# Kernel optimization log

Hardware: AMD Instinct MI355X
Metric: run time of the kernel (lower is better)

## Reference

```python
import jax, jax.numpy as jnp
import numpy as np

INNER_DIM = 512
SCALE = 1.0 / np.sqrt(INNER_DIM).astype(np.float32)  # module scales by 1/sqrt(inner_dim), not head_dim


def setup_inputs() -> dict:
    key = jax.random.key(0)
    ks = jax.random.split(key, 7)
    b, n, d = 4, 4096, 512
    s = 0.02
    return {
        "x": jax.random.normal(ks[0], (b, n, d), jnp.float32),
        "y": jax.random.normal(ks[1], (b, n, d), jnp.float32),
        "Wq": jax.random.normal(ks[2], (INNER_DIM, d), jnp.float32) * s,  # torch Linear weight [out, in]
        "Wk": jax.random.normal(ks[3], (INNER_DIM, d), jnp.float32) * s,
        "Wv": jax.random.normal(ks[4], (INNER_DIM, d), jnp.float32) * s,
        "Wo": jax.random.normal(ks[5], (d, INNER_DIM), jnp.float32) * s,
        "bo": jax.random.normal(ks[6], (d,), jnp.float32) * s,
    }


def reference(x, y, Wq, Wk, Wv, Wo, bo):
    # q, k from x; v from y (bias-free projections)
    q = jnp.einsum('bnd,id->bni', x, Wq)
    k = jnp.einsum('bnd,id->bni', x, Wk)
    v = jnp.einsum('bnd,id->bni', y, Wv)
    # full [b, n, n] scores, scaled by 1/sqrt(inner_dim)
    alpha = jnp.einsum('bik,bjk->bij', q, k) * SCALE
    alpha = jax.nn.softmax(alpha, axis=-1)
    ctx = jnp.einsum('bij,bjd->bid', alpha, v)
    out = jnp.einsum('bid,od->bio', ctx, Wo) + bo
    return out
```

## Files before the change

### kernel.cpp

```cpp
#include <hip/hip_runtime.h>
#include <hip/hip_bf16.h>


typedef unsigned short u16;
typedef __bf16 bf16x8 __attribute__((ext_vector_type(8)));
typedef float f32x4 __attribute__((ext_vector_type(4)));

#define SCALE_QK 0.044194173824159216f

__device__ __forceinline__ u16 f2bf(float f) {
    __hip_bfloat16 h = __float2bfloat16(f);
    return __builtin_bit_cast(u16, h);
}

__device__ __forceinline__ void load_lds16(const void* g, void* l) {
    __builtin_amdgcn_global_load_lds(
        (const __attribute__((address_space(1))) void*)g,
        (__attribute__((address_space(3))) void*)l, 16, 0, 0);
}

__global__ void cvt_bf16_kernel(const float* __restrict__ src, u16* __restrict__ dst,
                                int n8, float scale) {
    int i = blockIdx.x * blockDim.x + threadIdx.x;
    if (i >= n8) return;
    const float4* s4 = (const float4*)src;
    float4 v0 = s4[2 * i], v1 = s4[2 * i + 1];
    union { u16 u[8]; uint4 v; } o;
    o.u[0] = f2bf(v0.x * scale); o.u[1] = f2bf(v0.y * scale);
    o.u[2] = f2bf(v0.z * scale); o.u[3] = f2bf(v0.w * scale);
    o.u[4] = f2bf(v1.x * scale); o.u[5] = f2bf(v1.y * scale);
    o.u[6] = f2bf(v1.z * scale); o.u[7] = f2bf(v1.w * scale);
    ((uint4*)dst)[i] = o.v;
}

__global__ void wvo_kernel(const float* __restrict__ Wo, const float* __restrict__ Wv,
                           float* __restrict__ Wvo) {
    int o = blockIdx.x, t = threadIdx.x;
    float a0 = 0.f, a1 = 0.f;
    for (int i = 0; i < 512; ++i) {
        float w = Wo[o * 512 + i];
        a0 += w * Wv[i * 512 + t];
        a1 += w * Wv[i * 512 + t + 256];
    }
    Wvo[o * 512 + t] = a0;
    Wvo[o * 512 + t + 256] = a1;
}

__global__ void rowsum_kernel(const u16* __restrict__ P, float* __restrict__ l) {
    int row = blockIdx.x * 4 + (threadIdx.x >> 6);
    int lane = threadIdx.x & 63;
    const uint4* base = (const uint4*)(P + (size_t)row * 4096);
    float s = 0.f;
#pragma unroll
    for (int it = 0; it < 8; ++it) {
        uint4 c = base[it * 64 + lane];
        const u16* u = (const u16*)&c;
#pragma unroll
        for (int j = 0; j < 8; ++j)
            s += __uint_as_float(((unsigned)u[j]) << 16);
    }
#pragma unroll
    for (int off = 32; off > 0; off >>= 1) s += __shfl_xor(s, off, 64);
    if (lane == 0) l[row] = s;
}

template <int EPI>
__launch_bounds__(256)
__global__ void gemm_bt_kernel(const u16* __restrict__ A, const u16* __restrict__ B,
                               void* __restrict__ Cout, int N, int K,
                               long long sAz, long long sBz, long long sCz,
                               const float* __restrict__ lvec,
                               const float* __restrict__ bias) {
    __shared__ u16 As[2][128 * 32];
    __shared__ u16 Bs[2][128 * 32];

    const int tid = threadIdx.x;
    const int wave = tid >> 6, lane = tid & 63;
    const int lr = lane & 15, lg = lane >> 4;
    const int wr = wave >> 1, wc = wave & 1;
    const int z = blockIdx.z;
    const int row0 = blockIdx.y * 128, col0 = blockIdx.x * 128;

    const u16* Ab = A + (size_t)z * sAz;
    const u16* Bb = B + (size_t)z * sBz;

    f32x4 acc[4][4];
#pragma unroll
    for (int i = 0; i < 4; ++i)
#pragma unroll
        for (int j = 0; j < 4; ++j) acc[i][j] = (f32x4){0.f, 0.f, 0.f, 0.f};

    const int KT = K >> 5;

#define STAGE(bufi, kt2)                                                          \
    {                                                                             \
        _Pragma("unroll") for (int i = 0; i < 2; ++i) {                           \
            int chunk = i * 256 + tid;                                            \
            int r = chunk >> 2, c4 = chunk & 3;                                   \
            load_lds16(Ab + (size_t)(row0 + r) * K + (kt2) * 32 + c4 * 8,         \
                       &As[bufi][(i * 256 + wave * 64) * 8]);                     \
            load_lds16(Bb + (size_t)(col0 + r) * K + (kt2) * 32 + c4 * 8,         \
                       &Bs[bufi][(i * 256 + wave * 64) * 8]);                     \
        }                                                                         \
    }

    STAGE(0, 0);
    int buf = 0;
    for (int kt = 0; kt < KT; ++kt) {
        __syncthreads();
        if (kt + 1 < KT) STAGE(buf ^ 1, kt + 1);

        bf16x8 af[4], bfr[4];
#pragma unroll
        for (int mf = 0; mf < 4; ++mf)
            af[mf] = *(const bf16x8*)&As[buf][(wr * 64 + mf * 16 + lr) * 32 + lg * 8];
#pragma unroll
        for (int nf = 0; nf < 4; ++nf)
            bfr[nf] = *(const bf16x8*)&Bs[buf][(wc * 64 + nf * 16 + lr) * 32 + lg * 8];
#pragma unroll
        for (int mf = 0; mf < 4; ++mf)
#pragma unroll
            for (int nf = 0; nf < 4; ++nf)
                acc[mf][nf] = __builtin_amdgcn_mfma_f32_16x16x32_bf16(
                    af[mf], bfr[nf], acc[mf][nf], 0, 0, 0);
        buf ^= 1;
    }
#undef STAGE

    const int rbase = row0 + wr * 64;
    const int cbase = col0 + wc * 64;

    if (EPI == 0 || EPI == 2) {
        u16* C = (u16*)Cout + (size_t)z * sCz;
#pragma unroll
        for (int mf = 0; mf < 4; ++mf)
#pragma unroll
            for (int nf = 0; nf < 4; ++nf)
#pragma unroll
                for (int reg = 0; reg < 4; ++reg) {
                    int r = rbase + mf * 16 + lg * 4 + reg;
                    int c = cbase + nf * 16 + lr;
                    float v = acc[mf][nf][reg];
                    if (EPI == 2) v = __expf(v);
                    C[(size_t)r * N + c] = f2bf(v);
                }
    } else if (EPI == 1) {
        u16* C = (u16*)Cout;
#pragma unroll
        for (int mf = 0; mf < 4; ++mf)
#pragma unroll
            for (int nf = 0; nf < 4; ++nf) {
                int rg = rbase + mf * 16 + lg * 4;
                int bsel = rg >> 12, rl = rg & 4095;
                int c = cbase + nf * 16 + lr;
                union { u16 u[4]; uint2 v; } o;
#pragma unroll
                for (int reg = 0; reg < 4; ++reg) o.u[reg] = f2bf(acc[mf][nf][reg]);
                *(uint2*)(C + ((size_t)bsel << 21) + ((size_t)c << 12) + rl) = o.v;
            }
    } else {
        float* C = (float*)Cout + (size_t)z * sCz;
        const float* lz = lvec + z * 4096;
        float bo_c[4];
#pragma unroll
        for (int nf = 0; nf < 4; ++nf) bo_c[nf] = bias[cbase + nf * 16 + lr];
#pragma unroll
        for (int mf = 0; mf < 4; ++mf) {
            float4 lv = *(const float4*)&lz[rbase + mf * 16 + lg * 4];
            float inv[4] = {1.f / lv.x, 1.f / lv.y, 1.f / lv.z, 1.f / lv.w};
#pragma unroll
            for (int nf = 0; nf < 4; ++nf)
#pragma unroll
                for (int reg = 0; reg < 4; ++reg) {
                    int r = rbase + mf * 16 + lg * 4 + reg;
                    int c = cbase + nf * 16 + lr;
                    C[(size_t)r * N + c] = acc[mf][nf][reg] * inv[reg] + bo_c[nf];
                }
        }
    }
}

extern "C" void kernel_launch(void* const* d_in, const int* in_sizes, int n_in,
                              void* d_out, int out_size, void* d_ws, size_t ws_size,
                              hipStream_t stream) {
    const float* x  = (const float*)d_in[0];
    const float* y  = (const float*)d_in[1];
    const float* Wq = (const float*)d_in[2];
    const float* Wk = (const float*)d_in[3];
    const float* Wv = (const float*)d_in[4];
    const float* Wo = (const float*)d_in[5];
    const float* bo = (const float*)d_in[6];
    float* out = (float*)d_out;

    char* ws = (char*)d_ws;
    u16*   xb   = (u16*)(ws + 0);
    u16*   yb   = (u16*)(ws + 16777216);
    u16*   q    = (u16*)(ws + 33554432);
    u16*   k    = (u16*)(ws + 50331648);
    u16*   vwT  = (u16*)(ws + 67108864);
    u16*   Wqb  = (u16*)(ws + 83886080);
    u16*   Wkb  = (u16*)(ws + 84410368);
    u16*   Wvob = (u16*)(ws + 84934656);
    float* Wvo  = (float*)(ws + 85458944);
    float* lsum = (float*)(ws + 86507520);
    u16*   P    = (u16*)(ws + 86573056);

    cvt_bf16_kernel<<<4096, 256, 0, stream>>>(x, xb, 1048576, 1.0f);
    cvt_bf16_kernel<<<4096, 256, 0, stream>>>(y, yb, 1048576, 1.0f);
    cvt_bf16_kernel<<<128, 256, 0, stream>>>(Wq, Wqb, 32768, SCALE_QK);
    cvt_bf16_kernel<<<128, 256, 0, stream>>>(Wk, Wkb, 32768, 1.0f);

    wvo_kernel<<<512, 256, 0, stream>>>(Wo, Wv, Wvo);
    cvt_bf16_kernel<<<128, 256, 0, stream>>>(Wvo, Wvob, 32768, 1.0f);

    gemm_bt_kernel<0><<<dim3(4, 128, 1), 256, 0, stream>>>(xb, Wqb, q, 512, 512,
                                                           0, 0, 0, nullptr, nullptr);
    gemm_bt_kernel<0><<<dim3(4, 128, 1), 256, 0, stream>>>(xb, Wkb, k, 512, 512,
                                                           0, 0, 0, nullptr, nullptr);
    gemm_bt_kernel<1><<<dim3(4, 128, 1), 256, 0, stream>>>(yb, Wvob, vwT, 512, 512,
                                                           0, 0, 0, nullptr, nullptr);

    gemm_bt_kernel<2><<<dim3(32, 32, 4), 256, 0, stream>>>(q, k, P, 4096, 512,
                                                           2097152, 2097152, 16777216,
                                                           nullptr, nullptr);

    rowsum_kernel<<<4096, 256, 0, stream>>>(P, lsum);

    gemm_bt_kernel<3><<<dim3(4, 32, 4), 256, 0, stream>>>(P, vwT, out, 512, 4096,
                                                          16777216, 2097152, 2097152,
                                                          lsum, bo);
}
```

Baseline: 359.6 us.

## Fuse Q/K projections, fold rowsum into PV GEMM, add XCD-aware block remap

```diff
diff --git a/kernel.cpp b/kernel.cpp
--- a/kernel.cpp
+++ b/kernel.cpp
@@ -46,31 +46,11 @@
     Wvo[o * 512 + t + 256] = a1;
 }
 
-__global__ void rowsum_kernel(const u16* __restrict__ P, float* __restrict__ l) {
-    int row = blockIdx.x * 4 + (threadIdx.x >> 6);
-    int lane = threadIdx.x & 63;
-    const uint4* base = (const uint4*)(P + (size_t)row * 4096);
-    float s = 0.f;
-#pragma unroll
-    for (int it = 0; it < 8; ++it) {
-        uint4 c = base[it * 64 + lane];
-        const u16* u = (const u16*)&c;
-#pragma unroll
-        for (int j = 0; j < 8; ++j)
-            s += __uint_as_float(((unsigned)u[j]) << 16);
-    }
-#pragma unroll
-    for (int off = 32; off > 0; off >>= 1) s += __shfl_xor(s, off, 64);
-    if (lane == 0) l[row] = s;
-}
-
 template <int EPI>
 __launch_bounds__(256)
 __global__ void gemm_bt_kernel(const u16* __restrict__ A, const u16* __restrict__ B,
-                               void* __restrict__ Cout, int N, int K,
-                               long long sAz, long long sBz, long long sCz,
-                               const float* __restrict__ lvec,
-                               const float* __restrict__ bias) {
+                               void* __restrict__ Cout, int N, int K, int lda, int ldb,
+                               long long sAz, long long sBz, long long sCz) {
     __shared__ u16 As[2][128 * 32];
     __shared__ u16 Bs[2][128 * 32];
 
@@ -78,8 +58,15 @@
     const int wave = tid >> 6, lane = tid & 63;
     const int lr = lane & 15, lg = lane >> 4;
     const int wr = wave >> 1, wc = wave & 1;
-    const int z = blockIdx.z;
-    const int row0 = blockIdx.y * 128, col0 = blockIdx.x * 128;
+
+    const int gx = gridDim.x, gy = gridDim.y;
+    int bid = (blockIdx.z * gy + blockIdx.y) * gx + blockIdx.x;
+    const int nwg = gx * gy * gridDim.z;
+    int lgc = (bid & 7) * (nwg >> 3) + (bid >> 3);
+    const int bx = lgc % gx;
+    int rem = lgc / gx;
+    const int by = rem % gy, z = rem / gy;
+    const int row0 = by * 128, col0 = bx * 128;
 
     const u16* Ab = A + (size_t)z * sAz;
     const u16* Bb = B + (size_t)z * sBz;
@@ -97,9 +84,9 @@
         _Pragma("unroll") for (int i = 0; i < 2; ++i) {                           \
             int chunk = i * 256 + tid;                                            \
             int r = chunk >> 2, c4 = chunk & 3;                                   \
-            load_lds16(Ab + (size_t)(row0 + r) * K + (kt2) * 32 + c4 * 8,         \
+            load_lds16(Ab + (size_t)(row0 + r) * lda + (kt2) * 32 + c4 * 8,       \
                        &As[bufi][(i * 256 + wave * 64) * 8]);                     \
-            load_lds16(Bb + (size_t)(col0 + r) * K + (kt2) * 32 + c4 * 8,         \
+            load_lds16(Bb + (size_t)(col0 + r) * ldb + (kt2) * 32 + c4 * 8,       \
                        &Bs[bufi][(i * 256 + wave * 64) * 8]);                     \
         }                                                                         \
     }
@@ -144,7 +131,7 @@
                     if (EPI == 2) v = __expf(v);
                     C[(size_t)r * N + c] = f2bf(v);
                 }
-    } else if (EPI == 1) {
+    } else {
         u16* C = (u16*)Cout;
 #pragma unroll
         for (int mf = 0; mf < 4; ++mf)
@@ -158,24 +145,98 @@
                 for (int reg = 0; reg < 4; ++reg) o.u[reg] = f2bf(acc[mf][nf][reg]);
                 *(uint2*)(C + ((size_t)bsel << 21) + ((size_t)c << 12) + rl) = o.v;
             }
-    } else {
-        float* C = (float*)Cout + (size_t)z * sCz;
-        const float* lz = lvec + z * 4096;
-        float bo_c[4];
-#pragma unroll
-        for (int nf = 0; nf < 4; ++nf) bo_c[nf] = bias[cbase + nf * 16 + lr];
-#pragma unroll
-        for (int mf = 0; mf < 4; ++mf) {
-            float4 lv = *(const float4*)&lz[rbase + mf * 16 + lg * 4];
-            float inv[4] = {1.f / lv.x, 1.f / lv.y, 1.f / lv.z, 1.f / lv.w};
-#pragma unroll
-            for (int nf = 0; nf < 4; ++nf)
-#pragma unroll
-                for (int reg = 0; reg < 4; ++reg) {
-                    int r = rbase + mf * 16 + lg * 4 + reg;
-                    int c = cbase + nf * 16 + lr;
-                    C[(size_t)r * N + c] = acc[mf][nf][reg] * inv[reg] + bo_c[nf];
-                }
+    }
+}
+
+__launch_bounds__(512, 4)
+__global__ void pv_kernel(const u16* __restrict__ P, const u16* __restrict__ vwT,
+                          float* __restrict__ out, const float* __restrict__ bias) {
+    __shared__ u16 As[2][64 * 32];
+    __shared__ u16 Bs[2][512 * 32];
+    __shared__ float lsh[64];
+
+    const int tid = threadIdx.x;
+    const int wave = tid >> 6, lane = tid & 63;
+    const int lr = lane & 15, lg2 = lane >> 4;
+
+    int bid = blockIdx.y * 64 + blockIdx.x;
+    int lgc = (bid & 7) * 32 + (bid >> 3);
+    const int rowpanel = lgc & 63, z = lgc >> 6;
+    const int row0 = rowpanel * 64;
+
+    const u16* Pz = P + (size_t)z * 16777216;
+    const u16* Vz = vwT + (size_t)z * 2097152;
+    float* Oz = out + (size_t)z * 2097152 + (size_t)row0 * 512;
+
+    f32x4 acc[4][4];
+#pragma unroll
+    for (int i = 0; i < 4; ++i)
+#pragma unroll
+        for (int j = 0; j < 4; ++j) acc[i][j] = (f32x4){0.f, 0.f, 0.f, 0.f};
+    float rs = 0.f;
+
+#define STAGE(bufi, kt2)                                                          \
+    {                                                                             \
+        if (tid < 256) {                                                          \
+            int r = tid >> 2, c4 = tid & 3;                                       \
+            load_lds16(Pz + (size_t)(row0 + r) * 4096 + (kt2) * 32 + c4 * 8,      \
+                       &As[bufi][wave * 512]);                                    \
+        }                                                                         \
+        _Pragma("unroll") for (int it = 0; it < 4; ++it) {                        \
+            int c = it * 512 + tid;                                               \
+            int r = c >> 2, c4 = c & 3;                                           \
+            load_lds16(Vz + (size_t)r * 4096 + (kt2) * 32 + c4 * 8,               \
+                       &Bs[bufi][(it * 512 + wave * 64) * 8]);                    \
+        }                                                                         \
+    }
+
+    STAGE(0, 0);
+    int buf = 0;
+    for (int kt = 0; kt < 128; ++kt) {
+        __syncthreads();
+        if (kt + 1 < 128) STAGE(buf ^ 1, kt + 1);
+
+        {
+            uint2 rv = *(const uint2*)&As[buf][(tid >> 3) * 32 + (tid & 7) * 4];
+            rs += __uint_as_float(rv.x << 16) + __uint_as_float(rv.x & 0xffff0000u) +
+                  __uint_as_float(rv.y << 16) + __uint_as_float(rv.y & 0xffff0000u);
+        }
+
+        bf16x8 af[4];
+#pragma unroll
+        for (int mf = 0; mf < 4; ++mf)
+            af[mf] = *(const bf16x8*)&As[buf][(mf * 16 + lr) * 32 + lg2 * 8];
+#pragma unroll
+        for (int nf = 0; nf < 4; ++nf) {
+            bf16x8 bfr = *(const bf16x8*)&Bs[buf][(wave * 64 + nf * 16 + lr) * 32 + lg2 * 8];
+#pragma unroll
+            for (int mf = 0; mf < 4; ++mf)
+                acc[mf][nf] = __builtin_amdgcn_mfma_f32_16x16x32_bf16(
+                    af[mf], bfr, acc[mf][nf], 0, 0, 0);
+        }
+        buf ^= 1;
+    }
+#undef STAGE
+
+    rs += __shfl_xor(rs, 1, 64);
+    rs += __shfl_xor(rs, 2, 64);
+    rs += __shfl_xor(rs, 4, 64);
+    if ((tid & 7) == 0) lsh[tid >> 3] = rs;
+    __syncthreads();
+
+#pragma unroll
+    for (int mf = 0; mf < 4; ++mf) {
+        float4 lv = *(const float4*)&lsh[mf * 16 + lg2 * 4];
+        float inv[4] = {1.f / lv.x, 1.f / lv.y, 1.f / lv.z, 1.f / lv.w};
+#pragma unroll
+        for (int nf = 0; nf < 4; ++nf) {
+            int c = wave * 64 + nf * 16 + lr;
+            float b = bias[c];
+#pragma unroll
+            for (int reg = 0; reg < 4; ++reg) {
+                int r = mf * 16 + lg2 * 4 + reg;
+                Oz[(size_t)r * 512 + c] = acc[mf][nf][reg] * inv[reg] + b;
+            }
         }
     }
 }
@@ -195,38 +256,29 @@
     char* ws = (char*)d_ws;
     u16*   xb   = (u16*)(ws + 0);
     u16*   yb   = (u16*)(ws + 16777216);
-    u16*   q    = (u16*)(ws + 33554432);
-    u16*   k    = (u16*)(ws + 50331648);
+    u16*   qk   = (u16*)(ws + 33554432);
     u16*   vwT  = (u16*)(ws + 67108864);
-    u16*   Wqb  = (u16*)(ws + 83886080);
-    u16*   Wkb  = (u16*)(ws + 84410368);
+    u16*   Wqkb = (u16*)(ws + 83886080);
     u16*   Wvob = (u16*)(ws + 84934656);
     float* Wvo  = (float*)(ws + 85458944);
-    float* lsum = (float*)(ws + 86507520);
-    u16*   P    = (u16*)(ws + 86573056);
+    u16*   P    = (u16*)(ws + 86507520);
 
     cvt_bf16_kernel<<<4096, 256, 0, stream>>>(x, xb, 1048576, 1.0f);
     cvt_bf16_kernel<<<4096, 256, 0, stream>>>(y, yb, 1048576, 1.0f);
-    cvt_bf16_kernel<<<128, 256, 0, stream>>>(Wq, Wqb, 32768, SCALE_QK);
-    cvt_bf16_kernel<<<128, 256, 0, stream>>>(Wk, Wkb, 32768, 1.0f);
+    cvt_bf16_kernel<<<128, 256, 0, stream>>>(Wq, Wqkb, 32768, SCALE_QK);
+    cvt_bf16_kernel<<<128, 256, 0, stream>>>(Wk, Wqkb + 262144, 32768, 1.0f);
 
     wvo_kernel<<<512, 256, 0, stream>>>(Wo, Wv, Wvo);
     cvt_bf16_kernel<<<128, 256, 0, stream>>>(Wvo, Wvob, 32768, 1.0f);
 
-    gemm_bt_kernel<0><<<dim3(4, 128, 1), 256, 0, stream>>>(xb, Wqb, q, 512, 512,
-                                                           0, 0, 0, nullptr, nullptr);
-    gemm_bt_kernel<0><<<dim3(4, 128, 1), 256, 0, stream>>>(xb, Wkb, k, 512, 512,
-                                                           0, 0, 0, nullptr, nullptr);
-    gemm_bt_kernel<1><<<dim3(4, 128, 1), 256, 0, stream>>>(yb, Wvob, vwT, 512, 512,
-                                                           0, 0, 0, nullptr, nullptr);
-
-    gemm_bt_kernel<2><<<dim3(32, 32, 4), 256, 0, stream>>>(q, k, P, 4096, 512,
-                                                           2097152, 2097152, 16777216,
-                                                           nullptr, nullptr);
-
-    rowsum_kernel<<<4096, 256, 0, stream>>>(P, lsum);
-
-    gemm_bt_kernel<3><<<dim3(4, 32, 4), 256, 0, stream>>>(P, vwT, out, 512, 4096,
-                                                          16777216, 2097152, 2097152,
-                                                          lsum, bo);
-}
+    gemm_bt_kernel<0><<<dim3(8, 128, 1), 256, 0, stream>>>(xb, Wqkb, qk,
+                                                           1024, 512, 512, 512, 0, 0, 0);
+    gemm_bt_kernel<1><<<dim3(4, 128, 1), 256, 0, stream>>>(yb, Wvob, vwT,
+                                                           512, 512, 512, 512, 0, 0, 0);
+
+    gemm_bt_kernel<2><<<dim3(32, 32, 4), 256, 0, stream>>>(qk, qk + 512, P,
+                                                           4096, 512, 1024, 1024,
+                                                           4194304, 4194304, 16777216);
+
+    pv_kernel<<<dim3(64, 4, 1), 512, 0, stream>>>(P, vwT, out, bo);
+}
```

New measurement: 345.6 us. 3.9% less time.
